# Performance work log

Measured on AMD Instinct MI355X. Metric: run time of the kernel, lower is better.

Reference implementation:

```python
import jax, jax.numpy as jnp
import numpy as np
import math

NUM_LAYERS = 4
NHEAD = 8
D_MODEL = 256
EPS_ATTN = 1e-6
EPS_LN = 1e-5


def _pos_encoding(d_model, h, w, dtype):
    # LoFTR 2D sinusoidal pos-enc, sliced to (h, w)
    d4 = d_model // 4
    y_pos = jnp.arange(1, h + 1, dtype=dtype)[None, :, None]  # [1,h,1]
    x_pos = jnp.arange(1, w + 1, dtype=dtype)[None, None, :]  # [1,1,w]
    div = jnp.exp(jnp.arange(0, d_model // 2, 2, dtype=dtype) * (-math.log(10000.0) / (d_model // 2)))
    div = div[:, None, None]  # [d4,1,1]
    pe = jnp.zeros((d_model, h, w), dtype=dtype)
    pe = pe.at[0::4].set(jnp.sin(x_pos * div))
    pe = pe.at[1::4].set(jnp.cos(x_pos * div))
    pe = pe.at[2::4].set(jnp.sin(y_pos * div))
    pe = pe.at[3::4].set(jnp.cos(y_pos * div))
    return pe


def _layernorm(x, g, b):
    mu = jnp.mean(x, axis=-1, keepdims=True)
    var = jnp.mean(jnp.square(x - mu), axis=-1, keepdims=True)
    return (x - mu) * jax.lax.rsqrt(var + EPS_LN) * g + b


def _encoder_layer(x, Wq, Wk, Wv, Wm, W1, W2, g1, b1, g2, b2):
    # x: [n, L, d]; weights stored [in, out]
    n, L, d = x.shape
    dh = d // NHEAD
    q = (x @ Wq).reshape(n, L, NHEAD, dh)
    k = (x @ Wk).reshape(n, L, NHEAD, dh)
    v = (x @ Wv).reshape(n, L, NHEAD, dh)
    # linear attention: feature map elu(x)+1
    Q = jax.nn.elu(q) + 1.0
    K = jax.nn.elu(k) + 1.0
    v_len = jnp.asarray(L, x.dtype)
    V = v / v_len
    KV = jnp.einsum('nshd,nshv->nhdv', K, V)            # [n,H,dh,dh]
    Z = 1.0 / (jnp.einsum('nlhd,nhd->nlh', Q, K.sum(axis=1)) + EPS_ATTN)
    msg = jnp.einsum('nlhd,nhdv,nlh->nlhv', Q, KV, Z) * v_len  # [n,L,H,dh]
    msg = msg.reshape(n, L, d) @ Wm
    msg = _layernorm(msg, g1, b1)
    msg = jnp.concatenate([x, msg], axis=-1)             # [n,L,2d]
    msg = jax.nn.relu(msg @ W1) @ W2
    msg = _layernorm(msg, g2, b2)
    return x + msg


def setup_inputs() -> dict:
    key = jax.random.key(0)
    ks = jax.random.split(key, 8)
    b, c, h, w = 8, D_MODEL, 64, 64
    d = D_MODEL
    sc_d = 1.0 / math.sqrt(d)
    sc_2d = 1.0 / math.sqrt(2 * d)
    feats = jax.random.normal(ks[0], (b, c, h, w), dtype=jnp.float32)
    Wq = jax.random.normal(ks[1], (NUM_LAYERS, d, d), dtype=jnp.float32) * sc_d
    Wk = jax.random.normal(ks[2], (NUM_LAYERS, d, d), dtype=jnp.float32) * sc_d
    Wv = jax.random.normal(ks[3], (NUM_LAYERS, d, d), dtype=jnp.float32) * sc_d
    Wmerge = jax.random.normal(ks[4], (NUM_LAYERS, d, d), dtype=jnp.float32) * sc_d
    Wmlp1 = jax.random.normal(ks[5], (NUM_LAYERS, 2 * d, 2 * d), dtype=jnp.float32) * sc_2d
    Wmlp2 = jax.random.normal(ks[6], (NUM_LAYERS, 2 * d, d), dtype=jnp.float32) * sc_2d
    ln1_g = jnp.ones((NUM_LAYERS, d), dtype=jnp.float32)
    ln1_b = jnp.zeros((NUM_LAYERS, d), dtype=jnp.float32)
    ln2_g = jnp.ones((NUM_LAYERS, d), dtype=jnp.float32)
    ln2_b = jnp.zeros((NUM_LAYERS, d), dtype=jnp.float32)
    return {'feats': feats, 'Wq': Wq, 'Wk': Wk, 'Wv': Wv, 'Wmerge': Wmerge,
            'Wmlp1': Wmlp1, 'Wmlp2': Wmlp2, 'ln1_g': ln1_g, 'ln1_b': ln1_b,
            'ln2_g': ln2_g, 'ln2_b': ln2_b}


def reference(feats, Wq, Wk, Wv, Wmerge, Wmlp1, Wmlp2, ln1_g, ln1_b, ln2_g, ln2_b):
    b, c, h, w = feats.shape
    x = feats + _pos_encoding(c, h, w, feats.dtype)[None]   # add_posEnc=True
    x = x.reshape(b, c, h * w).transpose(0, 2, 1)            # n (h w) c
    for i in range(NUM_LAYERS):
        x = _encoder_layer(x, Wq[i], Wk[i], Wv[i], Wmerge[i], Wmlp1[i], Wmlp2[i],
                           ln1_g[i], ln1_b[i], ln2_g[i], ln2_b[i])
    return x.transpose(0, 2, 1).reshape(b, c, h, w)
```

## Files before the change

kernel.cpp:

```cpp
#include <hip/hip_runtime.h>
#include <hip/hip_bf16.h>

#define LTOT 4096
#define DM 256
#define BATCH 8
#define MROWS (BATCH * LTOT)
#define NX ((size_t)MROWS * DM)

typedef __bf16 bf16x8 __attribute__((ext_vector_type(8)));
typedef float f32x4 __attribute__((ext_vector_type(4)));

__device__ __forceinline__ float elu1(float x) {
    return x > 0.f ? x + 1.f : expf(x);
}
__device__ __forceinline__ ushort f2bf(float f) {
    unsigned u = __float_as_uint(f);
    u += 0x7FFFu + ((u >> 16) & 1u);
    return (ushort)(u >> 16);
}
__device__ __forceinline__ unsigned pkbf(float a, float b) {
    return (unsigned)f2bf(a) | ((unsigned)f2bf(b) << 16);
}
__device__ __forceinline__ float b2f(ushort u) {
    return __uint_as_float(((unsigned)u) << 16);
}

__global__ __launch_bounds__(256) void prep_kernel(const float* __restrict__ feats,
                                                   ushort* __restrict__ XC) {
    __shared__ float tile[32][33];
    int b = blockIdx.z;
    int l0 = blockIdx.x * 32;
    int c0 = blockIdx.y * 32;
    int tx = threadIdx.x, ty = threadIdx.y;
#pragma unroll
    for (int j = 0; j < 4; ++j) {
        int c = c0 + ty + j * 8;
        tile[ty + j * 8][tx] = feats[((size_t)(b * DM + c)) * LTOT + l0 + tx];
    }
    __syncthreads();
#pragma unroll
    for (int j = 0; j < 4; ++j) {
        int l = l0 + ty + j * 8;
        int c = c0 + tx;
        int i2 = (c >> 2) * 2;
        float dv = expf((float)i2 * -0.07195578415156063f);
        int rem = c & 3;
        int y = l >> 6, xc = l & 63;
        float pos = (rem < 2) ? (float)(xc + 1) : (float)(y + 1);
        float arg = pos * dv;
        float pe = (rem & 1) ? cosf(arg) : sinf(arg);
        float val = tile[tx][ty + j * 8] + pe;
        size_t row = (size_t)(b * LTOT + l);
        XC[row * 512 + c] = f2bf(val);
    }
}

__global__ __launch_bounds__(256) void unprep_kernel(const float* __restrict__ X,
                                                     float* __restrict__ out) {
    __shared__ float tile[32][33];
    int b = blockIdx.z;
    int l0 = blockIdx.x * 32;
    int c0 = blockIdx.y * 32;
    int tx = threadIdx.x, ty = threadIdx.y;
#pragma unroll
    for (int j = 0; j < 4; ++j) {
        int l = l0 + ty + j * 8;
        tile[ty + j * 8][tx] = X[((size_t)(b * LTOT + l)) * DM + c0 + tx];
    }
    __syncthreads();
#pragma unroll
    for (int j = 0; j < 4; ++j) {
        int c = c0 + ty + j * 8;
        out[((size_t)(b * DM + c)) * LTOT + l0 + tx] = tile[tx][ty + j * 8];
    }
}

__global__ __launch_bounds__(256) void wtrans_all(const float* __restrict__ Wq,
                                                  const float* __restrict__ Wk,
                                                  const float* __restrict__ Wv,
                                                  const float* __restrict__ Wm,
                                                  const float* __restrict__ W1,
                                                  const float* __restrict__ W2,
                                                  ushort* __restrict__ WTqkv,
                                                  ushort* __restrict__ WTm,
                                                  ushort* __restrict__ WT1,
                                                  ushort* __restrict__ WT2) {
    __shared__ float t[32][33];
    int idx = blockIdx.x;
    const float* W;
    ushort* WT;
    int K, N, KT, z, r;
    size_t in_ls, out_ls;
    if (idx < 1024) {
        int which = idx >> 8, local = idx & 255;
        K = 256; N = 256; KT = 8; in_ls = 65536;
        if (which == 0)      { W = Wq; WT = WTqkv;          out_ls = 196608; }
        else if (which == 1) { W = Wk; WT = WTqkv + 65536;  out_ls = 196608; }
        else if (which == 2) { W = Wv; WT = WTqkv + 131072; out_ls = 196608; }
        else                 { W = Wm; WT = WTm;            out_ls = 65536; }
        z = local >> 6; r = local & 63;
    } else if (idx < 2048) {
        int local = idx - 1024;
        K = 512; N = 512; KT = 16; in_ls = 262144; out_ls = 262144;
        W = W1; WT = WT1;
        z = local >> 8; r = local & 255;
    } else {
        int local = idx - 2048;
        K = 512; N = 256; KT = 16; in_ls = 131072; out_ls = 131072;
        W = W2; WT = WT2;
        z = local >> 7; r = local & 127;
    }
    int k0 = (r % KT) * 32, n0 = (r / KT) * 32;
    const float* Wz = W + (size_t)z * in_ls;
    ushort* WTz = WT + (size_t)z * out_ls;
    int tx = threadIdx.x & 31, ty = threadIdx.x >> 5;
#pragma unroll
    for (int j = 0; j < 4; ++j)
        t[ty + j * 8][tx] = Wz[(size_t)(k0 + ty + j * 8) * N + n0 + tx];
    __syncthreads();
#pragma unroll
    for (int j = 0; j < 4; ++j)
        WTz[(size_t)(n0 + ty + j * 8) * K + k0 + tx] = f2bf(t[tx][ty + j * 8]);
}

template <int ACT>
__global__ __launch_bounds__(256, 4) void gemm_bf16(const ushort* __restrict__ A, int lda,
                                                    const ushort* __restrict__ Bt,
                                                    ushort* __restrict__ Cb,
                                                    int N, int K) {
    __shared__ ushort As[4096];
    __shared__ ushort Bs[4096];
    int tid = threadIdx.x;
    int m0 = blockIdx.x * 128, n0 = blockIdx.y * 128;
    int wave = tid >> 6, lane = tid & 63;
    int wm = (wave >> 1) * 64, wn = (wave & 1) * 64;
    int fm = lane & 15, kg = lane >> 4;

    f32x4 acc[4][4] = {};

    for (int k0 = 0; k0 < K; k0 += 32) {
        const ushort* Ag = A + (size_t)m0 * lda + k0;
        const ushort* Bg = Bt + (size_t)n0 * K + k0;
#pragma unroll
        for (int iss = 0; iss < 2; ++iss) {
            int slot = iss * 256 + tid;
            int rr = slot >> 2, cc = (slot & 3) * 8;
            __builtin_amdgcn_global_load_lds(
                (const __attribute__((address_space(1))) void*)(Ag + (size_t)rr * lda + cc),
                (__attribute__((address_space(3))) void*)(As + iss * 2048 + wave * 512),
                16, 0, 0);
            __builtin_amdgcn_global_load_lds(
                (const __attribute__((address_space(1))) void*)(Bg + (size_t)rr * K + cc),
                (__attribute__((address_space(3))) void*)(Bs + iss * 2048 + wave * 512),
                16, 0, 0);
        }
        __syncthreads();
        bf16x8 afr[4], bfr[4];
#pragma unroll
        for (int i = 0; i < 4; ++i)
            afr[i] = *(const bf16x8*)(As + (wm + i * 16 + fm) * 32 + kg * 8);
#pragma unroll
        for (int j = 0; j < 4; ++j)
            bfr[j] = *(const bf16x8*)(Bs + (wn + j * 16 + fm) * 32 + kg * 8);
#pragma unroll
        for (int i = 0; i < 4; ++i)
#pragma unroll
            for (int j = 0; j < 4; ++j)
                acc[i][j] = __builtin_amdgcn_mfma_f32_16x16x32_bf16(afr[i], bfr[j], acc[i][j], 0, 0, 0);
        __syncthreads();
    }

#pragma unroll
    for (int i = 0; i < 4; ++i) {
        int grow0 = m0 + wm + i * 16 + kg * 4;
#pragma unroll
        for (int r = 0; r < 4; ++r) {
            size_t rowoff = (size_t)(grow0 + r) * N;
#pragma unroll
            for (int j = 0; j < 4; ++j) {
                float v = acc[i][j][r];
                int col = n0 + wn + j * 16 + fm;
                if (ACT == 2) v = fmaxf(v, 0.f);
                if (ACT == 3) v = (col < 512) ? elu1(v) : v;
                Cb[rowoff + col] = f2bf(v);
            }
        }
    }
}

template <int RES>
__global__ __launch_bounds__(256) void gemm_ln(const ushort* __restrict__ A, int lda,
                                               const ushort* __restrict__ Bt, int K,
                                               const float* __restrict__ g,
                                               const float* __restrict__ bta,
                                               float* __restrict__ Xout,
                                               ushort* __restrict__ XC) {
    __shared__ ushort As[2048];
    __shared__ ushort Bs[8192];
    __shared__ float red[64 * 8];
    __shared__ float musig[64 * 2];
    int tid = threadIdx.x;
    int m0 = blockIdx.x * 64;
    int wave = tid >> 6, lane = tid & 63;
    int wc = wave;
    int fm = lane & 15, kg = lane >> 4;

    f32x4 acc[4][4] = {};

    for (int k0 = 0; k0 < K; k0 += 32) {
        const ushort* Ag = A + (size_t)m0 * lda + k0;
        const ushort* Bg = Bt + k0;
        {
            int rr = tid >> 2, cc = (tid & 3) * 8;
            __builtin_amdgcn_global_load_lds(
                (const __attribute__((address_space(1))) void*)(Ag + (size_t)rr * lda + cc),
                (__attribute__((address_space(3))) void*)(As + wave * 512),
                16, 0, 0);
        }
#pragma unroll
        for (int iss = 0; iss < 4; ++iss) {
            int slot = iss * 256 + tid;
            int rr = slot >> 2, cc = (slot & 3) * 8;
            __builtin_amdgcn_global_load_lds(
                (const __attribute__((address_space(1))) void*)(Bg + (size_t)rr * K + cc),
                (__attribute__((address_space(3))) void*)(Bs + iss * 2048 + wave * 512),
                16, 0, 0);
        }
        __syncthreads();
        bf16x8 afr[4], bfr[4];
#pragma unroll
        for (int i = 0; i < 4; ++i)
            afr[i] = *(const bf16x8*)(As + (i * 16 + fm) * 32 + kg * 8);
#pragma unroll
        for (int j = 0; j < 4; ++j)
            bfr[j] = *(const bf16x8*)(Bs + (wc * 64 + j * 16 + fm) * 32 + kg * 8);
#pragma unroll
        for (int i = 0; i < 4; ++i)
#pragma unroll
            for (int j = 0; j < 4; ++j)
                acc[i][j] = __builtin_amdgcn_mfma_f32_16x16x32_bf16(afr[i], bfr[j], acc[i][j], 0, 0, 0);
        __syncthreads();
    }

#pragma unroll
    for (int i = 0; i < 4; ++i) {
#pragma unroll
        for (int r = 0; r < 4; ++r) {
            float s = acc[i][0][r] + acc[i][1][r] + acc[i][2][r] + acc[i][3][r];
            float q = acc[i][0][r] * acc[i][0][r] + acc[i][1][r] * acc[i][1][r] +
                      acc[i][2][r] * acc[i][2][r] + acc[i][3][r] * acc[i][3][r];
#pragma unroll
            for (int o = 1; o < 16; o <<= 1) {
                s += __shfl_xor(s, o, 64);
                q += __shfl_xor(q, o, 64);
            }
            if ((lane & 15) == 0) {
                int row = i * 16 + kg * 4 + r;
                red[row * 8 + wc] = s;
                red[row * 8 + 4 + wc] = q;
            }
        }
    }
    __syncthreads();
    if (tid < 64) {
        float s = red[tid * 8 + 0] + red[tid * 8 + 1] + red[tid * 8 + 2] + red[tid * 8 + 3];
        float q = red[tid * 8 + 4] + red[tid * 8 + 5] + red[tid * 8 + 6] + red[tid * 8 + 7];
        float mu = s * (1.f / 256.f);
        float var = q * (1.f / 256.f) - mu * mu;
        musig[tid * 2] = mu;
        musig[tid * 2 + 1] = rsqrtf(var + 1e-5f);
    }
    __syncthreads();

    float gv[4], bv[4];
#pragma unroll
    for (int j = 0; j < 4; ++j) {
        int col = wc * 64 + j * 16 + fm;
        gv[j] = g[col];
        bv[j] = bta[col];
    }
#pragma unroll
    for (int i = 0; i < 4; ++i) {
#pragma unroll
        for (int r = 0; r < 4; ++r) {
            int rl = i * 16 + kg * 4 + r;
            float mu = musig[rl * 2], rstd = musig[rl * 2 + 1];
            size_t grow = (size_t)(m0 + rl);
#pragma unroll
            for (int j = 0; j < 4; ++j) {
                int col = wc * 64 + j * 16 + fm;
                float v = (acc[i][j][r] - mu) * rstd * gv[j] + bv[j];
                if (RES) {
                    float x = b2f(XC[grow * 512 + col]) + v;
                    XC[grow * 512 + col] = f2bf(x);
                    if (Xout) Xout[grow * 256 + col] = x;
                } else {
                    XC[grow * 512 + 256 + col] = f2bf(v);
                }
            }
        }
    }
}

__global__ __launch_bounds__(256) void kv_kernel(const ushort* __restrict__ Kf,
                                                 const ushort* __restrict__ Vf,
                                                 int str,
                                                 float* __restrict__ KVp,
                                                 float* __restrict__ KSp) {
    __shared__ float redv[3][8][8][16];
    __shared__ float redk[3][8][4];
    int tid = threadIdx.x;
    int bh = blockIdx.x, sp = blockIdx.y;
    int b = bh >> 3, h = bh & 7;
    int sg = tid >> 6, d2 = (tid >> 3) & 7, v2 = tid & 7;
    size_t rbase = (size_t)(b * LTOT + sp * 512 + sg * 128) * str;
    const ushort* Kp = Kf + rbase + h * 32 + d2 * 4;
    const ushort* Vp = Vf + rbase + h * 32 + v2 * 4;
    float acc[4][4] = {};
    float ks[4] = {};
#pragma unroll 4
    for (int s = 0; s < 128; ++s) {
        ushort4 k4 = *(const ushort4*)(Kp + (size_t)s * str);
        ushort4 v4 = *(const ushort4*)(Vp + (size_t)s * str);
        float kk0 = b2f(k4.x), kk1 = b2f(k4.y), kk2 = b2f(k4.z), kk3 = b2f(k4.w);
        float vv0 = b2f(v4.x), vv1 = b2f(v4.y), vv2 = b2f(v4.z), vv3 = b2f(v4.w);
        acc[0][0] += kk0 * vv0; acc[0][1] += kk0 * vv1; acc[0][2] += kk0 * vv2; acc[0][3] += kk0 * vv3;
        acc[1][0] += kk1 * vv0; acc[1][1] += kk1 * vv1; acc[1][2] += kk1 * vv2; acc[1][3] += kk1 * vv3;
        acc[2][0] += kk2 * vv0; acc[2][1] += kk2 * vv1; acc[2][2] += kk2 * vv2; acc[2][3] += kk2 * vv3;
        acc[3][0] += kk3 * vv0; acc[3][1] += kk3 * vv1; acc[3][2] += kk3 * vv2; acc[3][3] += kk3 * vv3;
        ks[0] += kk0; ks[1] += kk1; ks[2] += kk2; ks[3] += kk3;
    }
    if (sg > 0) {
#pragma unroll
        for (int i = 0; i < 4; ++i)
#pragma unroll
            for (int j = 0; j < 4; ++j)
                redv[sg - 1][d2][v2][i * 4 + j] = acc[i][j];
        if (v2 == 0) {
#pragma unroll
            for (int i = 0; i < 4; ++i) redk[sg - 1][d2][i] = ks[i];
        }
    }
    __syncthreads();
    if (sg == 0) {
#pragma unroll
        for (int t = 0; t < 3; ++t)
#pragma unroll
            for (int i = 0; i < 4; ++i)
#pragma unroll
                for (int j = 0; j < 4; ++j)
                    acc[i][j] += redv[t][d2][v2][i * 4 + j];
        float* base = KVp + (size_t)(sp * 64 + bh) * 1024;
#pragma unroll
        for (int i = 0; i < 4; ++i) {
            float4 o = make_float4(acc[i][0], acc[i][1], acc[i][2], acc[i][3]);
            *(float4*)(base + (d2 * 4 + i) * 32 + v2 * 4) = o;
        }
        if (v2 == 0) {
#pragma unroll
            for (int t = 0; t < 3; ++t)
#pragma unroll
                for (int i = 0; i < 4; ++i) ks[i] += redk[t][d2][i];
#pragma unroll
            for (int i = 0; i < 4; ++i)
                KSp[(sp * 64 + bh) * 32 + d2 * 4 + i] = ks[i];
        }
    }
}

__global__ __launch_bounds__(256) void kvreduce_kernel(const float* __restrict__ KVp,
                                                       const float* __restrict__ KSp,
                                                       ushort* __restrict__ KVT,
                                                       float* __restrict__ KS) {
    int bh = blockIdx.x;
    int t = threadIdx.x;
    float4 s = make_float4(0.f, 0.f, 0.f, 0.f);
#pragma unroll
    for (int sp = 0; sp < 8; ++sp) {
        float4 v = *(const float4*)(KVp + ((size_t)(sp * 64 + bh)) * 1024 + t * 4);
        s.x += v.x; s.y += v.y; s.z += v.z; s.w += v.w;
    }
    int d = t >> 3, v0 = (t & 7) * 4;
    ushort* dst = KVT + (size_t)bh * 1024 + d;
    dst[(v0 + 0) * 32] = f2bf(s.x);
    dst[(v0 + 1) * 32] = f2bf(s.y);
    dst[(v0 + 2) * 32] = f2bf(s.z);
    dst[(v0 + 3) * 32] = f2bf(s.w);
    if (t < 32) {
        float ks = 0.f;
#pragma unroll
        for (int sp = 0; sp < 8; ++sp) ks += KSp[(sp * 64 + bh) * 32 + t];
        KS[bh * 32 + t] = ks;
    }
}

__global__ __launch_bounds__(256) void msg_mfma(const ushort* __restrict__ Qb, int qstr,
                                                const ushort* __restrict__ KVT,
                                                const float* __restrict__ KS,
                                                ushort* __restrict__ Msgb) {
    __shared__ ushort kvs[8 * 1280];
    int tid = threadIdx.x;
    int b = blockIdx.y;
    int lc = blockIdx.x;
    {
        const ushort* src = KVT + (size_t)b * 8192;
#pragma unroll
        for (int it = 0; it < 4; ++it) {
            int base = it * 2048 + tid * 8;
            int h = base >> 10, rem = base & 1023;
            int v = rem >> 5, d = rem & 31;
            bf16x8 val = *(const bf16x8*)(src + base);
            *(bf16x8*)(kvs + h * 1280 + v * 40 + d) = val;
        }
    }
    __syncthreads();
    int wave = tid >> 6, lane = tid & 63;
    int fm = lane & 15, kg = lane >> 4;
    int row0 = b * LTOT + lc * 64 + wave * 16;

    for (int h = 0; h < 8; ++h) {
        bf16x8 afr = *(const bf16x8*)(Qb + (size_t)(row0 + fm) * qstr + h * 32 + kg * 8);
        bf16x8 bfr0 = *(const bf16x8*)(kvs + h * 1280 + fm * 40 + kg * 8);
        bf16x8 bfr1 = *(const bf16x8*)(kvs + h * 1280 + (16 + fm) * 40 + kg * 8);
        f32x4 acc0 = {}, acc1 = {};
        acc0 = __builtin_amdgcn_mfma_f32_16x16x32_bf16(afr, bfr0, acc0, 0, 0, 0);
        acc1 = __builtin_amdgcn_mfma_f32_16x16x32_bf16(afr, bfr1, acc1, 0, 0, 0);
        const float* ksp = KS + (b * 8 + h) * 32 + kg * 8;
        float4 ka = *(const float4*)ksp;
        float4 kb = *(const float4*)(ksp + 4);
        float den = (float)afr[0] * ka.x + (float)afr[1] * ka.y +
                    (float)afr[2] * ka.z + (float)afr[3] * ka.w +
                    (float)afr[4] * kb.x + (float)afr[5] * kb.y +
                    (float)afr[6] * kb.z + (float)afr[7] * kb.w;
        den += __shfl_xor(den, 16, 64);
        den += __shfl_xor(den, 32, 64);
        float rz = 1.f / (den + 1e-6f);
#pragma unroll
        for (int r = 0; r < 4; ++r) {
            int rr = kg * 4 + r;
            float rzr = __shfl(rz, (kg << 4) | rr, 64);
            size_t ro = (size_t)(row0 + rr) * DM + h * 32;
            Msgb[ro + fm] = f2bf(acc0[r] * rzr);
            Msgb[ro + 16 + fm] = f2bf(acc1[r] * rzr);
        }
    }
}

extern "C" void kernel_launch(void* const* d_in, const int* in_sizes, int n_in,
                              void* d_out, int out_size, void* d_ws, size_t ws_size,
                              hipStream_t stream) {
    const float* feats = (const float*)d_in[0];
    const float* Wq = (const float*)d_in[1];
    const float* Wk = (const float*)d_in[2];
    const float* Wv = (const float*)d_in[3];
    const float* Wm = (const float*)d_in[4];
    const float* W1 = (const float*)d_in[5];
    const float* W2 = (const float*)d_in[6];
    const float* g1 = (const float*)d_in[7];
    const float* b1 = (const float*)d_in[8];
    const float* g2 = (const float*)d_in[9];
    const float* b2 = (const float*)d_in[10];

    float* ws = (float*)d_ws;
    float* X = ws;
    ushort* XC = (ushort*)(ws + NX);
    ushort* QKVb = (ushort*)(ws + 2 * NX);
    ushort* HBb = QKVb;

    float* dout = (float*)d_out;
    ushort* msgb = (ushort*)dout;
    ushort* WB = (ushort*)dout + NX;
    ushort* WTqkv = WB;
    ushort* WTm = WB + 4 * 196608;
    ushort* WT1 = WTm + 4 * 65536;
    ushort* WT2 = WT1 + 4 * 262144;
    float* KVp = dout + (NX + 2621440) / 2;
    float* KSp = KVp + 524288;
    ushort* KVT = (ushort*)(KSp + 16384);
    float* KS = (float*)(KVT + 65536);

    wtrans_all<<<2560, 256, 0, stream>>>(Wq, Wk, Wv, Wm, W1, W2, WTqkv, WTm, WT1, WT2);
    prep_kernel<<<dim3(128, 8, 8), dim3(32, 8), 0, stream>>>(feats, XC);

    for (int layer = 0; layer < 4; ++layer) {
        const ushort* wtqkv = WTqkv + (size_t)layer * 196608;
        const ushort* wtm = WTm + (size_t)layer * 65536;
        const ushort* wt1 = WT1 + (size_t)layer * 262144;
        const ushort* wt2 = WT2 + (size_t)layer * 131072;
        const float* lg1 = g1 + layer * DM;
        const float* lb1 = b1 + layer * DM;
        const float* lg2 = g2 + layer * DM;
        const float* lb2 = b2 + layer * DM;

        gemm_bf16<3><<<dim3(256, 6), 256, 0, stream>>>(XC, 512, wtqkv, QKVb, 768, 256);
        kv_kernel<<<dim3(64, 8), 256, 0, stream>>>(QKVb + 256, QKVb + 512, 768, KVp, KSp);
        kvreduce_kernel<<<64, 256, 0, stream>>>(KVp, KSp, KVT, KS);
        msg_mfma<<<dim3(64, 8), 256, 0, stream>>>(QKVb, 768, KVT, KS, msgb);
        gemm_ln<0><<<512, 256, 0, stream>>>(msgb, 256, wtm, 256, lg1, lb1, nullptr, XC);
        gemm_bf16<2><<<dim3(256, 4), 256, 0, stream>>>(XC, 512, wt1, HBb, 512, 512);
        gemm_ln<1><<<512, 256, 0, stream>>>(HBb, 512, wt2, 512, lg2, lb2,
                                            (layer == 3) ? X : nullptr, XC);
    }

    unprep_kernel<<<dim3(128, 8, 8), dim3(32, 8), 0, stream>>>(X, dout);
}
```

Baseline: 654.4 us.

## Double-buffer LDS tiles in bf16 GEMM and GEMM+LayerNorm kernels

Both GEMM kernels now keep two LDS buffers per operand. Each iteration issues the asynchronous global-to-LDS load for the next K-slice before the MFMAs on the current slice run, so memory latency can overlap with compute. This also removes one barrier per iteration. The cost is twice the shared-memory footprint per block, which may lower occupancy, especially in the LayerNorm-fused kernel.

```diff
diff --git a/kernel.cpp b/kernel.cpp
--- a/kernel.cpp
+++ b/kernel.cpp
@@ -128,47 +128,58 @@
                                                     const ushort* __restrict__ Bt,
                                                     ushort* __restrict__ Cb,
                                                     int N, int K) {
-    __shared__ ushort As[4096];
-    __shared__ ushort Bs[4096];
+    __shared__ ushort As[2][4096];
+    __shared__ ushort Bs[2][4096];
     int tid = threadIdx.x;
     int m0 = blockIdx.x * 128, n0 = blockIdx.y * 128;
     int wave = tid >> 6, lane = tid & 63;
     int wm = (wave >> 1) * 64, wn = (wave & 1) * 64;
     int fm = lane & 15, kg = lane >> 4;
+    int rr = tid >> 2, cc = (tid & 3) * 8;
+
+    const ushort* Ag = A + (size_t)m0 * lda;
+    const ushort* Bg = Bt + (size_t)n0 * K;
 
     f32x4 acc[4][4] = {};
 
+#define STAGE_G(buf, k0)                                                                     \
+    {                                                                                        \
+        const ushort* Ak = Ag + (k0);                                                        \
+        const ushort* Bk = Bg + (k0);                                                        \
+        _Pragma("unroll") for (int iss = 0; iss < 2; ++iss) {                                \
+            int r2 = rr + iss * 64;                                                          \
+            __builtin_amdgcn_global_load_lds(                                                \
+                (const __attribute__((address_space(1))) void*)(Ak + (size_t)r2 * lda + cc), \
+                (__attribute__((address_space(3))) void*)(&As[buf][iss * 2048 + wave * 512]),\
+                16, 0, 0);                                                                   \
+            __builtin_amdgcn_global_load_lds(                                                \
+                (const __attribute__((address_space(1))) void*)(Bk + (size_t)r2 * K + cc),   \
+                (__attribute__((address_space(3))) void*)(&Bs[buf][iss * 2048 + wave * 512]),\
+                16, 0, 0);                                                                   \
+        }                                                                                    \
+    }
+
+    STAGE_G(0, 0);
+    __syncthreads();
+    int cur = 0;
     for (int k0 = 0; k0 < K; k0 += 32) {
-        const ushort* Ag = A + (size_t)m0 * lda + k0;
-        const ushort* Bg = Bt + (size_t)n0 * K + k0;
-#pragma unroll
-        for (int iss = 0; iss < 2; ++iss) {
-            int slot = iss * 256 + tid;
-            int rr = slot >> 2, cc = (slot & 3) * 8;
-            __builtin_amdgcn_global_load_lds(
-                (const __attribute__((address_space(1))) void*)(Ag + (size_t)rr * lda + cc),
-                (__attribute__((address_space(3))) void*)(As + iss * 2048 + wave * 512),
-                16, 0, 0);
-            __builtin_amdgcn_global_load_lds(
-                (const __attribute__((address_space(1))) void*)(Bg + (size_t)rr * K + cc),
-                (__attribute__((address_space(3))) void*)(Bs + iss * 2048 + wave * 512),
-                16, 0, 0);
-        }
-        __syncthreads();
+        if (k0 + 32 < K) STAGE_G(cur ^ 1, k0 + 32);
         bf16x8 afr[4], bfr[4];
 #pragma unroll
         for (int i = 0; i < 4; ++i)
-            afr[i] = *(const bf16x8*)(As + (wm + i * 16 + fm) * 32 + kg * 8);
+            afr[i] = *(const bf16x8*)(&As[cur][(wm + i * 16 + fm) * 32 + kg * 8]);
 #pragma unroll
         for (int j = 0; j < 4; ++j)
-            bfr[j] = *(const bf16x8*)(Bs + (wn + j * 16 + fm) * 32 + kg * 8);
+            bfr[j] = *(const bf16x8*)(&Bs[cur][(wn + j * 16 + fm) * 32 + kg * 8]);
 #pragma unroll
         for (int i = 0; i < 4; ++i)
 #pragma unroll
             for (int j = 0; j < 4; ++j)
                 acc[i][j] = __builtin_amdgcn_mfma_f32_16x16x32_bf16(afr[i], bfr[j], acc[i][j], 0, 0, 0);
         __syncthreads();
-    }
+        cur ^= 1;
+    }
+#undef STAGE_G
 
 #pragma unroll
     for (int i = 0; i < 4; ++i) {
@@ -195,8 +206,8 @@
                                                const float* __restrict__ bta,
                                                float* __restrict__ Xout,
                                                ushort* __restrict__ XC) {
-    __shared__ ushort As[2048];
-    __shared__ ushort Bs[8192];
+    __shared__ ushort As[2][2048];
+    __shared__ ushort Bs[2][8192];
     __shared__ float red[64 * 8];
     __shared__ float musig[64 * 2];
     int tid = threadIdx.x;
@@ -204,43 +215,50 @@
     int wave = tid >> 6, lane = tid & 63;
     int wc = wave;
     int fm = lane & 15, kg = lane >> 4;
+    int rr = tid >> 2, cc = (tid & 3) * 8;
+
+    const ushort* Ag = A + (size_t)m0 * lda;
 
     f32x4 acc[4][4] = {};
 
+#define STAGE_L(buf, k0)                                                                     \
+    {                                                                                        \
+        const ushort* Ak = Ag + (k0);                                                        \
+        const ushort* Bk = Bt + (k0);                                                        \
+        __builtin_amdgcn_global_load_lds(                                                    \
+            (const __attribute__((address_space(1))) void*)(Ak + (size_t)rr * lda + cc),     \
+            (__attribute__((address_space(3))) void*)(&As[buf][wave * 512]),                 \
+            16, 0, 0);                                                                       \
+        _Pragma("unroll") for (int iss = 0; iss < 4; ++iss) {                                \
+            int r2 = rr + iss * 64;                                                          \
+            __builtin_amdgcn_global_load_lds(                                                \
+                (const __attribute__((address_space(1))) void*)(Bk + (size_t)r2 * K + cc),   \
+                (__attribute__((address_space(3))) void*)(&Bs[buf][iss * 2048 + wave * 512]),\
+                16, 0, 0);                                                                   \
+        }                                                                                    \
+    }
+
+    STAGE_L(0, 0);
+    __syncthreads();
+    int cur = 0;
     for (int k0 = 0; k0 < K; k0 += 32) {
-        const ushort* Ag = A + (size_t)m0 * lda + k0;
-        const ushort* Bg = Bt + k0;
-        {
-            int rr = tid >> 2, cc = (tid & 3) * 8;
-            __builtin_amdgcn_global_load_lds(
-                (const __attribute__((address_space(1))) void*)(Ag + (size_t)rr * lda + cc),
-                (__attribute__((address_space(3))) void*)(As + wave * 512),
-                16, 0, 0);
-        }
-#pragma unroll
-        for (int iss = 0; iss < 4; ++iss) {
-            int slot = iss * 256 + tid;
-            int rr = slot >> 2, cc = (slot & 3) * 8;
-            __builtin_amdgcn_global_load_lds(
-                (const __attribute__((address_space(1))) void*)(Bg + (size_t)rr * K + cc),
-                (__attribute__((address_space(3))) void*)(Bs + iss * 2048 + wave * 512),
-                16, 0, 0);
-        }
-        __syncthreads();
+        if (k0 + 32 < K) STAGE_L(cur ^ 1, k0 + 32);
         bf16x8 afr[4], bfr[4];
 #pragma unroll
         for (int i = 0; i < 4; ++i)
-            afr[i] = *(const bf16x8*)(As + (i * 16 + fm) * 32 + kg * 8);
+            afr[i] = *(const bf16x8*)(&As[cur][(i * 16 + fm) * 32 + kg * 8]);
 #pragma unroll
         for (int j = 0; j < 4; ++j)
-            bfr[j] = *(const bf16x8*)(Bs + (wc * 64 + j * 16 + fm) * 32 + kg * 8);
+            bfr[j] = *(const bf16x8*)(&Bs[cur][(wc * 64 + j * 16 + fm) * 32 + kg * 8]);
 #pragma unroll
         for (int i = 0; i < 4; ++i)
 #pragma unroll
             for (int j = 0; j < 4; ++j)
                 acc[i][j] = __builtin_amdgcn_mfma_f32_16x16x32_bf16(afr[i], bfr[j], acc[i][j], 0, 0, 0);
         __syncthreads();
-    }
+        cur ^= 1;
+    }
+#undef STAGE_L
 
 #pragma unroll
     for (int i = 0; i < 4; ++i) {
```

After: 661.9 us. No clear change (+1.1%).

## Triple-buffer GEMM LDS loads and enlarge tiles to 128x256 with 512 threads

Applied to the files above, without the earlier changes.

Both the plain bf16 GEMM and the GEMM+LayerNorm kernels now keep three LDS buffers and prefetch two K-steps ahead with global_load_lds. Each iteration waits on vmcnt and uses raw barriers instead of a full load-then-sync per step. Tiles grow to 128x256 per 512-thread block, with K made a template constant so the loop fully unrolls. The goal is to hide global load latency behind MFMA work and raise operand reuse per block, at the cost of fewer blocks in the grid and more LDS per block (about 72KB).

```diff
diff --git a/kernel.cpp b/kernel.cpp
--- a/kernel.cpp
+++ b/kernel.cpp
@@ -10,6 +10,9 @@
 typedef __bf16 bf16x8 __attribute__((ext_vector_type(8)));
 typedef float f32x4 __attribute__((ext_vector_type(4)));
 
+#define AS1 __attribute__((address_space(1)))
+#define AS3 __attribute__((address_space(3)))
+
 __device__ __forceinline__ float elu1(float x) {
     return x > 0.f ? x + 1.f : expf(x);
 }
@@ -17,9 +20,6 @@
     unsigned u = __float_as_uint(f);
     u += 0x7FFFu + ((u >> 16) & 1u);
     return (ushort)(u >> 16);
-}
-__device__ __forceinline__ unsigned pkbf(float a, float b) {
-    return (unsigned)f2bf(a) | ((unsigned)f2bf(b) << 16);
 }
 __device__ __forceinline__ float b2f(ushort u) {
     return __uint_as_float(((unsigned)u) << 16);
@@ -123,52 +123,65 @@
         WTz[(size_t)(n0 + ty + j * 8) * K + k0 + tx] = f2bf(t[tx][ty + j * 8]);
 }
 
-template <int ACT>
-__global__ __launch_bounds__(256, 4) void gemm_bf16(const ushort* __restrict__ A, int lda,
+template <int ACT, int K>
+__global__ __launch_bounds__(512, 2) void gemm_bf16(const ushort* __restrict__ A, int lda,
                                                     const ushort* __restrict__ Bt,
                                                     ushort* __restrict__ Cb,
-                                                    int N, int K) {
-    __shared__ ushort As[4096];
-    __shared__ ushort Bs[4096];
+                                                    int N) {
+    constexpr int S = K / 32;
+    __shared__ ushort As[3][4096];
+    __shared__ ushort Bs[3][8192];
     int tid = threadIdx.x;
-    int m0 = blockIdx.x * 128, n0 = blockIdx.y * 128;
+    int m0 = blockIdx.x * 128, n0 = blockIdx.y * 256;
     int wave = tid >> 6, lane = tid & 63;
-    int wm = (wave >> 1) * 64, wn = (wave & 1) * 64;
+    int wm = (wave >> 2) * 64, wn = (wave & 3) * 64;
     int fm = lane & 15, kg = lane >> 4;
+    int rr = tid >> 2, cc = (tid & 3) * 8;
+
+    const ushort* Ag = A + (size_t)(m0 + rr) * lda + cc;
+    const ushort* Bg = Bt + (size_t)(n0 + rr) * K + cc;
+    const ushort* Bg2 = Bt + (size_t)(n0 + rr + 128) * K + cc;
 
     f32x4 acc[4][4] = {};
 
-    for (int k0 = 0; k0 < K; k0 += 32) {
-        const ushort* Ag = A + (size_t)m0 * lda + k0;
-        const ushort* Bg = Bt + (size_t)n0 * K + k0;
-#pragma unroll
-        for (int iss = 0; iss < 2; ++iss) {
-            int slot = iss * 256 + tid;
-            int rr = slot >> 2, cc = (slot & 3) * 8;
-            __builtin_amdgcn_global_load_lds(
-                (const __attribute__((address_space(1))) void*)(Ag + (size_t)rr * lda + cc),
-                (__attribute__((address_space(3))) void*)(As + iss * 2048 + wave * 512),
-                16, 0, 0);
-            __builtin_amdgcn_global_load_lds(
-                (const __attribute__((address_space(1))) void*)(Bg + (size_t)rr * K + cc),
-                (__attribute__((address_space(3))) void*)(Bs + iss * 2048 + wave * 512),
-                16, 0, 0);
-        }
-        __syncthreads();
+#define STAGE_G(buf, k0)                                                          \
+    do {                                                                          \
+        __builtin_amdgcn_global_load_lds((const AS1 void*)(Ag + (k0)),            \
+                                         (AS3 void*)(&As[buf][wave * 512]),       \
+                                         16, 0, 0);                               \
+        __builtin_amdgcn_global_load_lds((const AS1 void*)(Bg + (k0)),            \
+                                         (AS3 void*)(&Bs[buf][wave * 512]),       \
+                                         16, 0, 0);                               \
+        __builtin_amdgcn_global_load_lds((const AS1 void*)(Bg2 + (k0)),           \
+                                         (AS3 void*)(&Bs[buf][4096 + wave * 512]),\
+                                         16, 0, 0);                               \
+    } while (0)
+
+    STAGE_G(0, 0);
+    STAGE_G(1, 32);
+#pragma unroll
+    for (int t = 0; t < S; ++t) {
+        if (t + 1 < S) asm volatile("s_waitcnt vmcnt(3)" ::: "memory");
+        else           asm volatile("s_waitcnt vmcnt(0)" ::: "memory");
+        __builtin_amdgcn_s_barrier();
+        const int rb = t % 3;
         bf16x8 afr[4], bfr[4];
 #pragma unroll
         for (int i = 0; i < 4; ++i)
-            afr[i] = *(const bf16x8*)(As + (wm + i * 16 + fm) * 32 + kg * 8);
+            afr[i] = *(const bf16x8*)(&As[rb][(wm + i * 16 + fm) * 32 + kg * 8]);
 #pragma unroll
         for (int j = 0; j < 4; ++j)
-            bfr[j] = *(const bf16x8*)(Bs + (wn + j * 16 + fm) * 32 + kg * 8);
+            bfr[j] = *(const bf16x8*)(&Bs[rb][(wn + j * 16 + fm) * 32 + kg * 8]);
+        if (t + 2 < S) STAGE_G((t + 2) % 3, (t + 2) * 32);
 #pragma unroll
         for (int i = 0; i < 4; ++i)
 #pragma unroll
             for (int j = 0; j < 4; ++j)
                 acc[i][j] = __builtin_amdgcn_mfma_f32_16x16x32_bf16(afr[i], bfr[j], acc[i][j], 0, 0, 0);
-        __syncthreads();
-    }
+        asm volatile("" ::: "memory");
+        __builtin_amdgcn_s_barrier();
+    }
+#undef STAGE_G
 
 #pragma unroll
     for (int i = 0; i < 4; ++i) {
@@ -188,59 +201,69 @@
     }
 }
 
-template <int RES>
-__global__ __launch_bounds__(256) void gemm_ln(const ushort* __restrict__ A, int lda,
-                                               const ushort* __restrict__ Bt, int K,
-                                               const float* __restrict__ g,
-                                               const float* __restrict__ bta,
-                                               float* __restrict__ Xout,
-                                               ushort* __restrict__ XC) {
-    __shared__ ushort As[2048];
-    __shared__ ushort Bs[8192];
-    __shared__ float red[64 * 8];
-    __shared__ float musig[64 * 2];
+template <int RES, int K>
+__global__ __launch_bounds__(512, 2) void gemm_ln(const ushort* __restrict__ A, int lda,
+                                                  const ushort* __restrict__ Bt,
+                                                  const float* __restrict__ g,
+                                                  const float* __restrict__ bta,
+                                                  float* __restrict__ Xout,
+                                                  ushort* __restrict__ XC) {
+    constexpr int S = K / 32;
+    __shared__ ushort As[3][4096];
+    __shared__ ushort Bs[3][8192];
+    __shared__ float red[128 * 8];
+    __shared__ float musig[128 * 2];
     int tid = threadIdx.x;
-    int m0 = blockIdx.x * 64;
+    int m0 = blockIdx.x * 128;
     int wave = tid >> 6, lane = tid & 63;
-    int wc = wave;
+    int wm = (wave >> 2) * 64, wn = (wave & 3) * 64;
     int fm = lane & 15, kg = lane >> 4;
+    int rr = tid >> 2, cc = (tid & 3) * 8;
+
+    const ushort* Ag = A + (size_t)(m0 + rr) * lda + cc;
+    const ushort* Bg = Bt + (size_t)rr * K + cc;
+    const ushort* Bg2 = Bt + (size_t)(rr + 128) * K + cc;
 
     f32x4 acc[4][4] = {};
 
-    for (int k0 = 0; k0 < K; k0 += 32) {
-        const ushort* Ag = A + (size_t)m0 * lda + k0;
-        const ushort* Bg = Bt + k0;
-        {
-            int rr = tid >> 2, cc = (tid & 3) * 8;
-            __builtin_amdgcn_global_load_lds(
-                (const __attribute__((address_space(1))) void*)(Ag + (size_t)rr * lda + cc),
-                (__attribute__((address_space(3))) void*)(As + wave * 512),
-                16, 0, 0);
-        }
-#pragma unroll
-        for (int iss = 0; iss < 4; ++iss) {
-            int slot = iss * 256 + tid;
-            int rr = slot >> 2, cc = (slot & 3) * 8;
-            __builtin_amdgcn_global_load_lds(
-                (const __attribute__((address_space(1))) void*)(Bg + (size_t)rr * K + cc),
-                (__attribute__((address_space(3))) void*)(Bs + iss * 2048 + wave * 512),
-                16, 0, 0);
-        }
-        __syncthreads();
+#define STAGE_L(buf, k0)                                                          \
+    do {                                                                          \
+        __builtin_amdgcn_global_load_lds((const AS1 void*)(Ag + (k0)),            \
+                                         (AS3 void*)(&As[buf][wave * 512]),       \
+                                         16, 0, 0);                               \
+        __builtin_amdgcn_global_load_lds((const AS1 void*)(Bg + (k0)),            \
+                                         (AS3 void*)(&Bs[buf][wave * 512]),       \
+                                         16, 0, 0);                               \
+        __builtin_amdgcn_global_load_lds((const AS1 void*)(Bg2 + (k0)),           \
+                                         (AS3 void*)(&Bs[buf][4096 + wave * 512]),\
+                                         16, 0, 0);                               \
+    } while (0)
+
+    STAGE_L(0, 0);
+    STAGE_L(1, 32);
+#pragma unroll
+    for (int t = 0; t < S; ++t) {
+        if (t + 1 < S) asm volatile("s_waitcnt vmcnt(3)" ::: "memory");
+        else           asm volatile("s_waitcnt vmcnt(0)" ::: "memory");
+        __builtin_amdgcn_s_barrier();
+        const int rb = t % 3;
         bf16x8 afr[4], bfr[4];
 #pragma unroll
         for (int i = 0; i < 4; ++i)
-            afr[i] = *(const bf16x8*)(As + (i * 16 + fm) * 32 + kg * 8);
+            afr[i] = *(const bf16x8*)(&As[rb][(wm + i * 16 + fm) * 32 + kg * 8]);
 #pragma unroll
         for (int j = 0; j < 4; ++j)
-            bfr[j] = *(const bf16x8*)(Bs + (wc * 64 + j * 16 + fm) * 32 + kg * 8);
+            bfr[j] = *(const bf16x8*)(&Bs[rb][(wn + j * 16 + fm) * 32 + kg * 8]);
+        if (t + 2 < S) STAGE_L((t + 2) % 3, (t + 2) * 32);
 #pragma unroll
         for (int i = 0; i < 4; ++i)
 #pragma unroll
             for (int j = 0; j < 4; ++j)
                 acc[i][j] = __builtin_amdgcn_mfma_f32_16x16x32_bf16(afr[i], bfr[j], acc[i][j], 0, 0, 0);
-        __syncthreads();
-    }
+        asm volatile("" ::: "memory");
+        __builtin_amdgcn_s_barrier();
+    }
+#undef STAGE_L
 
 #pragma unroll
     for (int i = 0; i < 4; ++i) {
@@ -255,14 +278,14 @@
                 q += __shfl_xor(q, o, 64);
             }
             if ((lane & 15) == 0) {
-                int row = i * 16 + kg * 4 + r;
-                red[row * 8 + wc] = s;
-                red[row * 8 + 4 + wc] = q;
+                int row = wm + i * 16 + kg * 4 + r;
+                red[row * 8 + (wave & 3)] = s;
+                red[row * 8 + 4 + (wave & 3)] = q;
             }
         }
     }
     __syncthreads();
-    if (tid < 64) {
+    if (tid < 128) {
         float s = red[tid * 8 + 0] + red[tid * 8 + 1] + red[tid * 8 + 2] + red[tid * 8 + 3];
         float q = red[tid * 8 + 4] + red[tid * 8 + 5] + red[tid * 8 + 6] + red[tid * 8 + 7];
         float mu = s * (1.f / 256.f);
@@ -275,7 +298,7 @@
     float gv[4], bv[4];
 #pragma unroll
     for (int j = 0; j < 4; ++j) {
-        int col = wc * 64 + j * 16 + fm;
+        int col = wn + j * 16 + fm;
         gv[j] = g[col];
         bv[j] = bta[col];
     }
@@ -283,12 +306,12 @@
     for (int i = 0; i < 4; ++i) {
 #pragma unroll
         for (int r = 0; r < 4; ++r) {
-            int rl = i * 16 + kg * 4 + r;
+            int rl = wm + i * 16 + kg * 4 + r;
             float mu = musig[rl * 2], rstd = musig[rl * 2 + 1];
             size_t grow = (size_t)(m0 + rl);
 #pragma unroll
             for (int j = 0; j < 4; ++j) {
-                int col = wc * 64 + j * 16 + fm;
+                int col = wn + j * 16 + fm;
                 float v = (acc[i][j][r] - mu) * rstd * gv[j] + bv[j];
                 if (RES) {
                     float x = b2f(XC[grow * 512 + col]) + v;
@@ -492,14 +515,14 @@
         const float* lg2 = g2 + layer * DM;
         const float* lb2 = b2 + layer * DM;
 
-        gemm_bf16<3><<<dim3(256, 6), 256, 0, stream>>>(XC, 512, wtqkv, QKVb, 768, 256);
+        gemm_bf16<3, 256><<<dim3(256, 3), 512, 0, stream>>>(XC, 512, wtqkv, QKVb, 768);
         kv_kernel<<<dim3(64, 8), 256, 0, stream>>>(QKVb + 256, QKVb + 512, 768, KVp, KSp);
         kvreduce_kernel<<<64, 256, 0, stream>>>(KVp, KSp, KVT, KS);
         msg_mfma<<<dim3(64, 8), 256, 0, stream>>>(QKVb, 768, KVT, KS, msgb);
-        gemm_ln<0><<<512, 256, 0, stream>>>(msgb, 256, wtm, 256, lg1, lb1, nullptr, XC);
-        gemm_bf16<2><<<dim3(256, 4), 256, 0, stream>>>(XC, 512, wt1, HBb, 512, 512);
-        gemm_ln<1><<<512, 256, 0, stream>>>(HBb, 512, wt2, 512, lg2, lb2,
-                                            (layer == 3) ? X : nullptr, XC);
+        gemm_ln<0, 256><<<256, 512, 0, stream>>>(msgb, 256, wtm, lg1, lb1, nullptr, XC);
+        gemm_bf16<2, 512><<<dim3(256, 2), 512, 0, stream>>>(XC, 512, wt1, HBb, 512);
+        gemm_ln<1, 512><<<256, 512, 0, stream>>>(HBb, 512, wt2, lg2, lb2,
+                                                 (layer == 3) ? X : nullptr, XC);
     }
 
     unprep_kernel<<<dim3(128, 8, 8), dim3(32, 8), 0, stream>>>(X, dout);
```

Result: faster. 626.0 us (-4.3%).

## Unify GEMMs into 256x256-tile double-buffered kernel with swizzled LDS and fused LayerNorm

Applied to the files above, without the earlier changes.

Replaces the two GEMM kernels (128x128 tiles, and 64-row LayerNorm variants) with one templated 512-thread kernel that computes 256x256 output tiles. It uses K-chunks of 64, double-buffers global-to-LDS loads across iterations, and applies an XOR-style swizzle to cut LDS bank conflicts. The LayerNorm and residual epilogues are folded in as modes. The aim is more data reuse per tile, hiding load latency and fewer barriers per FLOP. In exchange it uses 128KB of LDS per block and many accumulator registers, and launches far fewer blocks (128–384), which may leave the 256 CUs underfilled.

```diff
diff --git a/kernel.cpp b/kernel.cpp
--- a/kernel.cpp
+++ b/kernel.cpp
@@ -10,6 +10,9 @@
 typedef __bf16 bf16x8 __attribute__((ext_vector_type(8)));
 typedef float f32x4 __attribute__((ext_vector_type(4)));
 
+#define AS1 __attribute__((address_space(1)))
+#define AS3 __attribute__((address_space(3)))
+
 __device__ __forceinline__ float elu1(float x) {
     return x > 0.f ? x + 1.f : expf(x);
 }
@@ -17,9 +20,6 @@
     unsigned u = __float_as_uint(f);
     u += 0x7FFFu + ((u >> 16) & 1u);
     return (ushort)(u >> 16);
-}
-__device__ __forceinline__ unsigned pkbf(float a, float b) {
-    return (unsigned)f2bf(a) | ((unsigned)f2bf(b) << 16);
 }
 __device__ __forceinline__ float b2f(ushort u) {
     return __uint_as_float(((unsigned)u) << 16);
@@ -123,179 +123,155 @@
         WTz[(size_t)(n0 + ty + j * 8) * K + k0 + tx] = f2bf(t[tx][ty + j * 8]);
 }
 
-template <int ACT>
-__global__ __launch_bounds__(256, 4) void gemm_bf16(const ushort* __restrict__ A, int lda,
-                                                    const ushort* __restrict__ Bt,
-                                                    ushort* __restrict__ Cb,
-                                                    int N, int K) {
-    __shared__ ushort As[4096];
-    __shared__ ushort Bs[4096];
+template <int MODE, int K>
+__global__ __launch_bounds__(512, 2) void gemm8(const ushort* __restrict__ A, int lda,
+                                                const ushort* __restrict__ Bt, int N,
+                                                ushort* __restrict__ Cb,
+                                                const float* __restrict__ g,
+                                                const float* __restrict__ bta,
+                                                float* __restrict__ Xout,
+                                                ushort* __restrict__ XC) {
+    constexpr int NT = K / 64;
+    __shared__ ushort arena[65536];
     int tid = threadIdx.x;
-    int m0 = blockIdx.x * 128, n0 = blockIdx.y * 128;
+    int m0 = blockIdx.x * 256;
+    int n0 = blockIdx.y * 256;
     int wave = tid >> 6, lane = tid & 63;
-    int wm = (wave >> 1) * 64, wn = (wave & 1) * 64;
+    int wm = (wave >> 2) * 128, wn = (wave & 3) * 64;
     int fm = lane & 15, kg = lane >> 4;
 
-    f32x4 acc[4][4] = {};
-
-    for (int k0 = 0; k0 < K; k0 += 32) {
-        const ushort* Ag = A + (size_t)m0 * lda + k0;
-        const ushort* Bg = Bt + (size_t)n0 * K + k0;
-#pragma unroll
-        for (int iss = 0; iss < 2; ++iss) {
-            int slot = iss * 256 + tid;
-            int rr = slot >> 2, cc = (slot & 3) * 8;
-            __builtin_amdgcn_global_load_lds(
-                (const __attribute__((address_space(1))) void*)(Ag + (size_t)rr * lda + cc),
-                (__attribute__((address_space(3))) void*)(As + iss * 2048 + wave * 512),
-                16, 0, 0);
-            __builtin_amdgcn_global_load_lds(
-                (const __attribute__((address_space(1))) void*)(Bg + (size_t)rr * K + cc),
-                (__attribute__((address_space(3))) void*)(Bs + iss * 2048 + wave * 512),
-                16, 0, 0);
+    int w8 = wave * 8 + (lane >> 3);
+    int cs = (((lane & 7) - (lane >> 3)) & 7) * 8;
+    const ushort* Asrc = A + (size_t)(m0 + w8) * lda + cs;
+    const ushort* Bsrc = Bt + (size_t)(n0 + w8) * K + cs;
+    const int ls0 = ((kg + fm) & 7) * 8;
+    const int ls1 = ((4 + kg + fm) & 7) * 8;
+
+    f32x4 acc[8][4] = {};
+
+#define STAGE8(buf, kt)                                                               \
+    do {                                                                              \
+        _Pragma("unroll") for (int i = 0; i < 4; ++i) {                               \
+            __builtin_amdgcn_global_load_lds(                                         \
+                (const AS1 void*)(Asrc + (size_t)(i * 64) * lda + (kt) * 64),         \
+                (AS3 void*)(arena + (buf) * 32768 + i * 4096 + wave * 512), 16, 0, 0);\
+            __builtin_amdgcn_global_load_lds(                                         \
+                (const AS1 void*)(Bsrc + (size_t)(i * 64) * K + (kt) * 64),           \
+                (AS3 void*)(arena + (buf) * 32768 + 16384 + i * 4096 + wave * 512),   \
+                16, 0, 0);                                                            \
+        }                                                                             \
+    } while (0)
+
+    STAGE8(0, 0);
+    if (NT > 1) STAGE8(1, 1);
+#pragma unroll
+    for (int kt = 0; kt < NT; ++kt) {
+        if (kt == 0) asm volatile("s_waitcnt vmcnt(8)" ::: "memory");
+        else         asm volatile("s_waitcnt vmcnt(0)" ::: "memory");
+        __builtin_amdgcn_s_barrier();
+        asm volatile("" ::: "memory");
+        if (kt >= 1 && kt + 1 < NT) STAGE8((kt + 1) & 1, kt + 1);
+        const ushort* Ab = arena + (kt & 1) * 32768 + (wm + fm) * 64;
+        const ushort* Bb = arena + (kt & 1) * 32768 + 16384 + (wn + fm) * 64;
+        bf16x8 bfr[4][2];
+#pragma unroll
+        for (int nj = 0; nj < 4; ++nj) {
+            bfr[nj][0] = *(const bf16x8*)(Bb + nj * 1024 + ls0);
+            bfr[nj][1] = *(const bf16x8*)(Bb + nj * 1024 + ls1);
+        }
+#pragma unroll
+        for (int q = 0; q < 4; ++q) {
+            bf16x8 a00 = *(const bf16x8*)(Ab + (2 * q) * 1024 + ls0);
+            bf16x8 a01 = *(const bf16x8*)(Ab + (2 * q) * 1024 + ls1);
+            bf16x8 a10 = *(const bf16x8*)(Ab + (2 * q + 1) * 1024 + ls0);
+            bf16x8 a11 = *(const bf16x8*)(Ab + (2 * q + 1) * 1024 + ls1);
+            __builtin_amdgcn_s_setprio(1);
+#pragma unroll
+            for (int nj = 0; nj < 4; ++nj) {
+                acc[2 * q][nj] = __builtin_amdgcn_mfma_f32_16x16x32_bf16(a00, bfr[nj][0], acc[2 * q][nj], 0, 0, 0);
+                acc[2 * q][nj] = __builtin_amdgcn_mfma_f32_16x16x32_bf16(a01, bfr[nj][1], acc[2 * q][nj], 0, 0, 0);
+                acc[2 * q + 1][nj] = __builtin_amdgcn_mfma_f32_16x16x32_bf16(a10, bfr[nj][0], acc[2 * q + 1][nj], 0, 0, 0);
+                acc[2 * q + 1][nj] = __builtin_amdgcn_mfma_f32_16x16x32_bf16(a11, bfr[nj][1], acc[2 * q + 1][nj], 0, 0, 0);
+            }
+            __builtin_amdgcn_s_setprio(0);
+        }
+    }
+#undef STAGE8
+
+    if (MODE <= 1) {
+#pragma unroll
+        for (int mi = 0; mi < 8; ++mi) {
+            int grow0 = m0 + wm + mi * 16 + kg * 4;
+#pragma unroll
+            for (int r = 0; r < 4; ++r) {
+                size_t rowoff = (size_t)(grow0 + r) * N;
+#pragma unroll
+                for (int nj = 0; nj < 4; ++nj) {
+                    float v = acc[mi][nj][r];
+                    int col = n0 + wn + nj * 16 + fm;
+                    if (MODE == 1) v = fmaxf(v, 0.f);
+                    if (MODE == 0) v = (col < 512) ? elu1(v) : v;
+                    Cb[rowoff + col] = f2bf(v);
+                }
+            }
+        }
+    } else {
+        float* red = (float*)arena;
+        float* musig = ((float*)arena) + 2048;
+#pragma unroll
+        for (int mi = 0; mi < 8; ++mi) {
+#pragma unroll
+            for (int r = 0; r < 4; ++r) {
+                float s = acc[mi][0][r] + acc[mi][1][r] + acc[mi][2][r] + acc[mi][3][r];
+                float q = acc[mi][0][r] * acc[mi][0][r] + acc[mi][1][r] * acc[mi][1][r] +
+                          acc[mi][2][r] * acc[mi][2][r] + acc[mi][3][r] * acc[mi][3][r];
+#pragma unroll
+                for (int o = 1; o < 16; o <<= 1) {
+                    s += __shfl_xor(s, o, 64);
+                    q += __shfl_xor(q, o, 64);
+                }
+                if ((lane & 15) == 0) {
+                    int rl = wm + mi * 16 + kg * 4 + r;
+                    red[rl * 8 + (wave & 3)] = s;
+                    red[rl * 8 + 4 + (wave & 3)] = q;
+                }
+            }
         }
         __syncthreads();
-        bf16x8 afr[4], bfr[4];
-#pragma unroll
-        for (int i = 0; i < 4; ++i)
-            afr[i] = *(const bf16x8*)(As + (wm + i * 16 + fm) * 32 + kg * 8);
-#pragma unroll
-        for (int j = 0; j < 4; ++j)
-            bfr[j] = *(const bf16x8*)(Bs + (wn + j * 16 + fm) * 32 + kg * 8);
-#pragma unroll
-        for (int i = 0; i < 4; ++i)
-#pragma unroll
-            for (int j = 0; j < 4; ++j)
-                acc[i][j] = __builtin_amdgcn_mfma_f32_16x16x32_bf16(afr[i], bfr[j], acc[i][j], 0, 0, 0);
+        if (tid < 256) {
+            float s = red[tid * 8 + 0] + red[tid * 8 + 1] + red[tid * 8 + 2] + red[tid * 8 + 3];
+            float q = red[tid * 8 + 4] + red[tid * 8 + 5] + red[tid * 8 + 6] + red[tid * 8 + 7];
+            float mu = s * (1.f / 256.f);
+            float var = q * (1.f / 256.f) - mu * mu;
+            musig[tid * 2] = mu;
+            musig[tid * 2 + 1] = rsqrtf(var + 1e-5f);
+        }
         __syncthreads();
-    }
-
-#pragma unroll
-    for (int i = 0; i < 4; ++i) {
-        int grow0 = m0 + wm + i * 16 + kg * 4;
-#pragma unroll
-        for (int r = 0; r < 4; ++r) {
-            size_t rowoff = (size_t)(grow0 + r) * N;
-#pragma unroll
-            for (int j = 0; j < 4; ++j) {
-                float v = acc[i][j][r];
-                int col = n0 + wn + j * 16 + fm;
-                if (ACT == 2) v = fmaxf(v, 0.f);
-                if (ACT == 3) v = (col < 512) ? elu1(v) : v;
-                Cb[rowoff + col] = f2bf(v);
-            }
-        }
-    }
-}
-
-template <int RES>
-__global__ __launch_bounds__(256) void gemm_ln(const ushort* __restrict__ A, int lda,
-                                               const ushort* __restrict__ Bt, int K,
-                                               const float* __restrict__ g,
-                                               const float* __restrict__ bta,
-                                               float* __restrict__ Xout,
-                                               ushort* __restrict__ XC) {
-    __shared__ ushort As[2048];
-    __shared__ ushort Bs[8192];
-    __shared__ float red[64 * 8];
-    __shared__ float musig[64 * 2];
-    int tid = threadIdx.x;
-    int m0 = blockIdx.x * 64;
-    int wave = tid >> 6, lane = tid & 63;
-    int wc = wave;
-    int fm = lane & 15, kg = lane >> 4;
-
-    f32x4 acc[4][4] = {};
-
-    for (int k0 = 0; k0 < K; k0 += 32) {
-        const ushort* Ag = A + (size_t)m0 * lda + k0;
-        const ushort* Bg = Bt + k0;
-        {
-            int rr = tid >> 2, cc = (tid & 3) * 8;
-            __builtin_amdgcn_global_load_lds(
-                (const __attribute__((address_space(1))) void*)(Ag + (size_t)rr * lda + cc),
-                (__attribute__((address_space(3))) void*)(As + wave * 512),
-                16, 0, 0);
-        }
-#pragma unroll
-        for (int iss = 0; iss < 4; ++iss) {
-            int slot = iss * 256 + tid;
-            int rr = slot >> 2, cc = (slot & 3) * 8;
-            __builtin_amdgcn_global_load_lds(
-                (const __attribute__((address_space(1))) void*)(Bg + (size_t)rr * K + cc),
-                (__attribute__((address_space(3))) void*)(Bs + iss * 2048 + wave * 512),
-                16, 0, 0);
-        }
-        __syncthreads();
-        bf16x8 afr[4], bfr[4];
-#pragma unroll
-        for (int i = 0; i < 4; ++i)
-            afr[i] = *(const bf16x8*)(As + (i * 16 + fm) * 32 + kg * 8);
-#pragma unroll
-        for (int j = 0; j < 4; ++j)
-            bfr[j] = *(const bf16x8*)(Bs + (wc * 64 + j * 16 + fm) * 32 + kg * 8);
-#pragma unroll
-        for (int i = 0; i < 4; ++i)
-#pragma unroll
-            for (int j = 0; j < 4; ++j)
-                acc[i][j] = __builtin_amdgcn_mfma_f32_16x16x32_bf16(afr[i], bfr[j], acc[i][j], 0, 0, 0);
-        __syncthreads();
-    }
-
-#pragma unroll
-    for (int i = 0; i < 4; ++i) {
-#pragma unroll
-        for (int r = 0; r < 4; ++r) {
-            float s = acc[i][0][r] + acc[i][1][r] + acc[i][2][r] + acc[i][3][r];
-            float q = acc[i][0][r] * acc[i][0][r] + acc[i][1][r] * acc[i][1][r] +
-                      acc[i][2][r] * acc[i][2][r] + acc[i][3][r] * acc[i][3][r];
-#pragma unroll
-            for (int o = 1; o < 16; o <<= 1) {
-                s += __shfl_xor(s, o, 64);
-                q += __shfl_xor(q, o, 64);
-            }
-            if ((lane & 15) == 0) {
-                int row = i * 16 + kg * 4 + r;
-                red[row * 8 + wc] = s;
-                red[row * 8 + 4 + wc] = q;
-            }
-        }
-    }
-    __syncthreads();
-    if (tid < 64) {
-        float s = red[tid * 8 + 0] + red[tid * 8 + 1] + red[tid * 8 + 2] + red[tid * 8 + 3];
-        float q = red[tid * 8 + 4] + red[tid * 8 + 5] + red[tid * 8 + 6] + red[tid * 8 + 7];
-        float mu = s * (1.f / 256.f);
-        float var = q * (1.f / 256.f) - mu * mu;
-        musig[tid * 2] = mu;
-        musig[tid * 2 + 1] = rsqrtf(var + 1e-5f);
-    }
-    __syncthreads();
-
-    float gv[4], bv[4];
-#pragma unroll
-    for (int j = 0; j < 4; ++j) {
-        int col = wc * 64 + j * 16 + fm;
-        gv[j] = g[col];
-        bv[j] = bta[col];
-    }
-#pragma unroll
-    for (int i = 0; i < 4; ++i) {
-#pragma unroll
-        for (int r = 0; r < 4; ++r) {
-            int rl = i * 16 + kg * 4 + r;
-            float mu = musig[rl * 2], rstd = musig[rl * 2 + 1];
-            size_t grow = (size_t)(m0 + rl);
-#pragma unroll
-            for (int j = 0; j < 4; ++j) {
-                int col = wc * 64 + j * 16 + fm;
-                float v = (acc[i][j][r] - mu) * rstd * gv[j] + bv[j];
-                if (RES) {
-                    float x = b2f(XC[grow * 512 + col]) + v;
-                    XC[grow * 512 + col] = f2bf(x);
-                    if (Xout) Xout[grow * 256 + col] = x;
-                } else {
-                    XC[grow * 512 + 256 + col] = f2bf(v);
+        float gv[4], bv[4];
+#pragma unroll
+        for (int nj = 0; nj < 4; ++nj) {
+            int col = wn + nj * 16 + fm;
+            gv[nj] = g[col];
+            bv[nj] = bta[col];
+        }
+#pragma unroll
+        for (int mi = 0; mi < 8; ++mi) {
+#pragma unroll
+            for (int r = 0; r < 4; ++r) {
+                int rl = wm + mi * 16 + kg * 4 + r;
+                float mu = musig[rl * 2], rstd = musig[rl * 2 + 1];
+                size_t grow = (size_t)(m0 + rl);
+#pragma unroll
+                for (int nj = 0; nj < 4; ++nj) {
+                    int col = wn + nj * 16 + fm;
+                    float v = (acc[mi][nj][r] - mu) * rstd * gv[nj] + bv[nj];
+                    if (MODE == 3) {
+                        float x = b2f(XC[grow * 512 + col]) + v;
+                        XC[grow * 512 + col] = f2bf(x);
+                        if (Xout) Xout[grow * 256 + col] = x;
+                    } else {
+                        XC[grow * 512 + 256 + col] = f2bf(v);
+                    }
                 }
             }
         }
@@ -492,14 +468,17 @@
         const float* lg2 = g2 + layer * DM;
         const float* lb2 = b2 + layer * DM;
 
-        gemm_bf16<3><<<dim3(256, 6), 256, 0, stream>>>(XC, 512, wtqkv, QKVb, 768, 256);
+        gemm8<0, 256><<<dim3(128, 3), 512, 0, stream>>>(XC, 512, wtqkv, 768, QKVb,
+                                                        nullptr, nullptr, nullptr, nullptr);
         kv_kernel<<<dim3(64, 8), 256, 0, stream>>>(QKVb + 256, QKVb + 512, 768, KVp, KSp);
         kvreduce_kernel<<<64, 256, 0, stream>>>(KVp, KSp, KVT, KS);
         msg_mfma<<<dim3(64, 8), 256, 0, stream>>>(QKVb, 768, KVT, KS, msgb);
-        gemm_ln<0><<<512, 256, 0, stream>>>(msgb, 256, wtm, 256, lg1, lb1, nullptr, XC);
-        gemm_bf16<2><<<dim3(256, 4), 256, 0, stream>>>(XC, 512, wt1, HBb, 512, 512);
-        gemm_ln<1><<<512, 256, 0, stream>>>(HBb, 512, wt2, 512, lg2, lb2,
-                                            (layer == 3) ? X : nullptr, XC);
+        gemm8<2, 256><<<dim3(128, 1), 512, 0, stream>>>(msgb, 256, wtm, 256, nullptr,
+                                                        lg1, lb1, nullptr, XC);
+        gemm8<1, 512><<<dim3(128, 2), 512, 0, stream>>>(XC, 512, wt1, 512, HBb,
+                                                        nullptr, nullptr, nullptr, nullptr);
+        gemm8<3, 512><<<dim3(128, 1), 512, 0, stream>>>(HBb, 512, wt2, 256, nullptr,
+                                                        lg2, lb2, (layer == 3) ? X : nullptr, XC);
     }
 
     unprep_kernel<<<dim3(128, 8, 8), dim3(32, 8), 0, stream>>>(X, dout);
```

After: 736.7 us. 1.13x slower.
